# Optimization experiments

Measured on AMD Instinct MI355X. Metric: run time of the kernel, lower is better.

Reference implementation:

```python
import jax, jax.numpy as jnp
import numpy as np

L, D, H, d = 16, 1024, 16, 64
NB, BS = 1024, 16        # num physical blocks, block size (tokens per block)
START_POS = 16368        # T = START_POS + L = 16384
SCALE = 1.0 / np.sqrt(d)


def setup_inputs() -> dict:
    key = jax.random.key(0)
    ks = jax.random.split(key, 5)
    return {
        "x": jax.random.normal(ks[0], (L, D), jnp.float32),
        "k_pool": jax.random.normal(ks[1], (NB, BS, H, d), jnp.float32),
        "v_pool": jax.random.normal(ks[2], (NB, BS, H, d), jnp.float32),
        "W_attn": jax.random.normal(ks[3], (D, 3 * D), jnp.float32) * 0.02,
        "b_attn": jnp.zeros((3 * D,), jnp.float32),
        "W_proj": jax.random.normal(ks[4], (D, D), jnp.float32) * 0.02,
        "b_proj": jnp.zeros((D,), jnp.float32),
        "block_ids": jnp.arange(NB, dtype=jnp.int64),
        "start_pos": START_POS,
    }


def reference(x, k_pool, v_pool, W_attn, b_attn, W_proj, b_proj, block_ids, start_pos):
    # QKV projection
    qkv = x @ W_attn + b_attn                      # [L, 3D]
    q, k, v = jnp.split(qkv, 3, axis=-1)
    q = q.reshape(L, H, d)
    k = k.reshape(L, H, d)
    v = v.reshape(L, H, d)

    # paged write of new K/V into the pool
    pos = start_pos + jnp.arange(L)                # logical positions of new tokens
    blk = block_ids[pos // BS]                     # physical block per token
    off = pos % BS
    k_pool = k_pool.at[blk, off].set(k)
    v_pool = v_pool.at[blk, off].set(v)

    # paged read of the full prefix [0, T)
    T = start_pos + L
    k_pos = jnp.arange(T)
    kb = block_ids[k_pos // BS]
    ko = k_pos % BS
    k_cache = k_pool[kb, ko]                       # [T, H, d]
    v_cache = v_pool[kb, ko]                       # [T, H, d]

    # attention: scores [H, L, T]
    scores = jnp.einsum("lhd,thd->hlt", q, k_cache) * SCALE
    mask = k_pos[None, :] > pos[:, None]           # [L, T] future positions
    scores = jnp.where(mask[None, :, :], -jnp.inf, scores)
    attn = jax.nn.softmax(scores.astype(jnp.float32), axis=-1).astype(scores.dtype)

    out = jnp.einsum("hlt,thd->lhd", attn, v_cache).reshape(L, D)
    return out @ W_proj + b_proj
```

## Files before the change

### kernel.cpp

```cpp
#include <hip/hip_runtime.h>
#include <math.h>

#define L_TOK 16
#define DMODEL 1024
#define NHEAD 16
#define DHEAD 64
#define NBLK 1024
#define BSZ 16
#define START_POS_C 16368
#define TTOT 16384
#define SPLITS 128
#define CHUNK 128
#define KSPLIT 16
#define QSCALE (0.125f * 1.4426950408889634f)

#define OFF_QKVP 0
#define OFF_QW   (OFF_QKVP + KSPLIT * L_TOK * 3 * DMODEL)
#define OFF_ACC  (OFF_QW + NHEAD * L_TOK * DHEAD)
#define OFF_M    (OFF_ACC + NHEAD * SPLITS * L_TOK * DHEAD)
#define OFF_SE   (OFF_M + NHEAD * SPLITS * L_TOK)
#define OFF_ATTN (OFF_SE + NHEAD * SPLITS * L_TOK)
#define OFF_PROJP (OFF_ATTN + L_TOK * DMODEL)

typedef _Float16 half2_t __attribute__((ext_vector_type(2)));
typedef _Float16 half4_t __attribute__((ext_vector_type(4)));
typedef _Float16 half8_t __attribute__((ext_vector_type(8)));
typedef float float4v __attribute__((ext_vector_type(4)));

union H8 { _Float16 h[8]; half8_t v; };
union H4 { _Float16 h[4]; half4_t v; };

__global__ __launch_bounds__(256) void gemm_part(const float* __restrict__ x,
                                                 const float* __restrict__ W,
                                                 float* __restrict__ part,
                                                 int ncols) {
    const int lane = threadIdx.x & 63;
    const int wv = threadIdx.x >> 6;
    const int n = blockIdx.x * 64 + lane;
    const int k0 = blockIdx.y * (DMODEL / KSPLIT);
    const float* xr = x + (size_t)(wv * 4) * DMODEL;
    float a0 = 0.f, a1 = 0.f, a2 = 0.f, a3 = 0.f;
#pragma unroll 8
    for (int k = k0; k < k0 + DMODEL / KSPLIT; ++k) {
        float w = W[(size_t)k * ncols + n];
        a0 = fmaf(xr[k], w, a0);
        a1 = fmaf(xr[DMODEL + k], w, a1);
        a2 = fmaf(xr[2 * DMODEL + k], w, a2);
        a3 = fmaf(xr[3 * DMODEL + k], w, a3);
    }
    size_t base = ((size_t)blockIdx.y * L_TOK + wv * 4) * ncols + n;
    part[base] = a0;
    part[base + (size_t)ncols] = a1;
    part[base + 2 * (size_t)ncols] = a2;
    part[base + 3 * (size_t)ncols] = a3;
}

__global__ __launch_bounds__(256) void qkv_reduce_scatter(const float* __restrict__ part,
                                                          const float* __restrict__ b_attn,
                                                          const int* __restrict__ block_ids,
                                                          float* __restrict__ qws,
                                                          float* __restrict__ kpool,
                                                          float* __restrict__ vpool) {
    int tid = blockIdx.x * 256 + threadIdx.x;
    int n = tid % (3 * DMODEL);
    int l = tid / (3 * DMODEL);
    float s = b_attn[n];
#pragma unroll
    for (int kb = 0; kb < KSPLIT; ++kb)
        s += part[((size_t)kb * L_TOK + l) * (3 * DMODEL) + n];
    int sec = n >> 10;
    int m = n & (DMODEL - 1);
    int h = m >> 6;
    int dd = m & 63;
    if (sec == 0) {
        qws[(h * L_TOK + l) * DHEAD + dd] = s * QSCALE;
    } else {
        int pos = START_POS_C + l;
        int blk = block_ids[pos >> 4];
        int off = pos & 15;
        size_t idx = (((size_t)blk * BSZ + off) * NHEAD + h) * DHEAD + dd;
        if (sec == 1) kpool[idx] = s;
        else          vpool[idx] = s;
    }
}

__global__ __launch_bounds__(64) void paged_attn(const float* __restrict__ kpool,
                                                 const float* __restrict__ vpool,
                                                 const int* __restrict__ block_ids,
                                                 const float* __restrict__ qws,
                                                 float* __restrict__ accws,
                                                 float* __restrict__ m_arr,
                                                 float* __restrict__ se_arr) {
    const int h = blockIdx.x;
    const int s = blockIdx.y;
    const int lane = threadIdx.x;
    const int c = lane & 15;
    const int quad = lane >> 4;

    __shared__ float VT[2][64][36];

    H8 qb0, qb1;
    {
        const float* qr = qws + ((size_t)(h * L_TOK + c)) * DHEAD + quad * 8;
        float4 q0 = *(const float4*)(qr);
        float4 q1 = *(const float4*)(qr + 4);
        float4 q2 = *(const float4*)(qr + 32);
        float4 q3 = *(const float4*)(qr + 36);
        qb0.h[0] = (_Float16)q0.x; qb0.h[1] = (_Float16)q0.y;
        qb0.h[2] = (_Float16)q0.z; qb0.h[3] = (_Float16)q0.w;
        qb0.h[4] = (_Float16)q1.x; qb0.h[5] = (_Float16)q1.y;
        qb0.h[6] = (_Float16)q1.z; qb0.h[7] = (_Float16)q1.w;
        qb1.h[0] = (_Float16)q2.x; qb1.h[1] = (_Float16)q2.y;
        qb1.h[2] = (_Float16)q2.z; qb1.h[3] = (_Float16)q2.w;
        qb1.h[4] = (_Float16)q3.x; qb1.h[5] = (_Float16)q3.y;
        qb1.h[6] = (_Float16)q3.z; qb1.h[7] = (_Float16)q3.w;
    }

    float4v acc[4];
#pragma unroll
    for (int i = 0; i < 4; ++i) acc[i] = (float4v){0.f, 0.f, 0.f, 0.f};
    float m_run = -INFINITY, se_run = 0.f;

    const int blk0 = s * (CHUNK / 16);

#pragma unroll 2
    for (int grp = 0; grp < CHUNK / 32; ++grp) {
        const int tb = s * CHUNK + grp * 32;
        const int buf = grp & 1;
        const int pb0 = block_ids[blk0 + 2 * grp];
        const int pb1 = block_ids[blk0 + 2 * grp + 1];

        const float* kr0 = kpool + (((size_t)pb0 * BSZ + c) * NHEAD + h) * DHEAD + quad * 8;
        const float* kr1 = kpool + (((size_t)pb1 * BSZ + c) * NHEAD + h) * DHEAD + quad * 8;
        const float* vr0 = vpool + (((size_t)pb0 * BSZ + c) * NHEAD + h) * DHEAD + quad * 8;
        const float* vr1 = vpool + (((size_t)pb1 * BSZ + c) * NHEAD + h) * DHEAD + quad * 8;
        float4 k0a = *(const float4*)(kr0);      float4 k0b = *(const float4*)(kr0 + 4);
        float4 k0c = *(const float4*)(kr0 + 32); float4 k0d = *(const float4*)(kr0 + 36);
        float4 k1a = *(const float4*)(kr1);      float4 k1b = *(const float4*)(kr1 + 4);
        float4 k1c = *(const float4*)(kr1 + 32); float4 k1d = *(const float4*)(kr1 + 36);
        float4 v0a = *(const float4*)(vr0);      float4 v0b = *(const float4*)(vr0 + 4);
        float4 v0c = *(const float4*)(vr0 + 32); float4 v0d = *(const float4*)(vr0 + 36);
        float4 v1a = *(const float4*)(vr1);      float4 v1b = *(const float4*)(vr1 + 4);
        float4 v1c = *(const float4*)(vr1 + 32); float4 v1d = *(const float4*)(vr1 + 36);

        {
            float* w0 = &VT[buf][quad * 8][c];
            w0[0*36]=v0a.x; w0[1*36]=v0a.y; w0[2*36]=v0a.z; w0[3*36]=v0a.w;
            w0[4*36]=v0b.x; w0[5*36]=v0b.y; w0[6*36]=v0b.z; w0[7*36]=v0b.w;
            float* w1 = &VT[buf][32 + quad * 8][c];
            w1[0*36]=v0c.x; w1[1*36]=v0c.y; w1[2*36]=v0c.z; w1[3*36]=v0c.w;
            w1[4*36]=v0d.x; w1[5*36]=v0d.y; w1[6*36]=v0d.z; w1[7*36]=v0d.w;
            float* w2 = &VT[buf][quad * 8][16 + c];
            w2[0*36]=v1a.x; w2[1*36]=v1a.y; w2[2*36]=v1a.z; w2[3*36]=v1a.w;
            w2[4*36]=v1b.x; w2[5*36]=v1b.y; w2[6*36]=v1b.z; w2[7*36]=v1b.w;
            float* w3 = &VT[buf][32 + quad * 8][16 + c];
            w3[0*36]=v1c.x; w3[1*36]=v1c.y; w3[2*36]=v1c.z; w3[3*36]=v1c.w;
            w3[4*36]=v1d.x; w3[5*36]=v1d.y; w3[6*36]=v1d.z; w3[7*36]=v1d.w;
        }

        const float4v z4 = {0.f, 0.f, 0.f, 0.f};
        H8 ka, kb;
        ka.h[0]=(_Float16)k0a.x; ka.h[1]=(_Float16)k0a.y; ka.h[2]=(_Float16)k0a.z; ka.h[3]=(_Float16)k0a.w;
        ka.h[4]=(_Float16)k0b.x; ka.h[5]=(_Float16)k0b.y; ka.h[6]=(_Float16)k0b.z; ka.h[7]=(_Float16)k0b.w;
        kb.h[0]=(_Float16)k0c.x; kb.h[1]=(_Float16)k0c.y; kb.h[2]=(_Float16)k0c.z; kb.h[3]=(_Float16)k0c.w;
        kb.h[4]=(_Float16)k0d.x; kb.h[5]=(_Float16)k0d.y; kb.h[6]=(_Float16)k0d.z; kb.h[7]=(_Float16)k0d.w;
        float4v st0 = __builtin_amdgcn_mfma_f32_16x16x32_f16(ka.v, qb0.v, z4, 0, 0, 0);
        st0 = __builtin_amdgcn_mfma_f32_16x16x32_f16(kb.v, qb1.v, st0, 0, 0, 0);
        ka.h[0]=(_Float16)k1a.x; ka.h[1]=(_Float16)k1a.y; ka.h[2]=(_Float16)k1a.z; ka.h[3]=(_Float16)k1a.w;
        ka.h[4]=(_Float16)k1b.x; ka.h[5]=(_Float16)k1b.y; ka.h[6]=(_Float16)k1b.z; ka.h[7]=(_Float16)k1b.w;
        kb.h[0]=(_Float16)k1c.x; kb.h[1]=(_Float16)k1c.y; kb.h[2]=(_Float16)k1c.z; kb.h[3]=(_Float16)k1c.w;
        kb.h[4]=(_Float16)k1d.x; kb.h[5]=(_Float16)k1d.y; kb.h[6]=(_Float16)k1d.z; kb.h[7]=(_Float16)k1d.w;
        float4v st1 = __builtin_amdgcn_mfma_f32_16x16x32_f16(ka.v, qb0.v, z4, 0, 0, 0);
        st1 = __builtin_amdgcn_mfma_f32_16x16x32_f16(kb.v, qb1.v, st1, 0, 0, 0);

        if (tb + 31 > START_POS_C) {
#pragma unroll
            for (int r = 0; r < 4; ++r) {
                if (tb + 4 * quad + r > START_POS_C + c)      st0[r] = -INFINITY;
                if (tb + 16 + 4 * quad + r > START_POS_C + c) st1[r] = -INFINITY;
            }
        }

        float tm = fmaxf(fmaxf(fmaxf(st0[0], st0[1]), fmaxf(st0[2], st0[3])),
                         fmaxf(fmaxf(st1[0], st1[1]), fmaxf(st1[2], st1[3])));
        tm = fmaxf(tm, __shfl_xor(tm, 16, 64));
        tm = fmaxf(tm, __shfl_xor(tm, 32, 64));
        const float m_new = fmaxf(m_run, tm);
        const float alpha = exp2f(m_run - m_new);
        float p[8];
        p[0] = exp2f(st0[0] - m_new); p[1] = exp2f(st0[1] - m_new);
        p[2] = exp2f(st0[2] - m_new); p[3] = exp2f(st0[3] - m_new);
        p[4] = exp2f(st1[0] - m_new); p[5] = exp2f(st1[1] - m_new);
        p[6] = exp2f(st1[2] - m_new); p[7] = exp2f(st1[3] - m_new);
        H4 pa0, pa1;
        pa0.h[0]=(_Float16)p[0]; pa0.h[1]=(_Float16)p[1];
        pa0.h[2]=(_Float16)p[2]; pa0.h[3]=(_Float16)p[3];
        pa1.h[0]=(_Float16)p[4]; pa1.h[1]=(_Float16)p[5];
        pa1.h[2]=(_Float16)p[6]; pa1.h[3]=(_Float16)p[7];
        float ts = ((float)pa0.h[0] + (float)pa0.h[1]) + ((float)pa0.h[2] + (float)pa0.h[3])
                 + ((float)pa1.h[0] + (float)pa1.h[1]) + ((float)pa1.h[2] + (float)pa1.h[3]);
        ts += __shfl_xor(ts, 16, 64);
        ts += __shfl_xor(ts, 32, 64);
        se_run = se_run * alpha + ts;
        m_run = m_new;

        float ar[4];
#pragma unroll
        for (int r = 0; r < 4; ++r) ar[r] = __shfl(alpha, quad * 4 + r, 64);
#pragma unroll
        for (int ndv = 0; ndv < 4; ++ndv)
#pragma unroll
            for (int r = 0; r < 4; ++r) acc[ndv][r] *= ar[r];

#pragma unroll
        for (int tau = 0; tau < 2; ++tau) {
            const half4_t pf = tau ? pa1.v : pa0.v;
#pragma unroll
            for (int ndv = 0; ndv < 4; ++ndv) {
                float4 vb = *(const float4*)&VT[buf][16 * ndv + c][16 * tau + 4 * quad];
                H4 bf;
                bf.h[0] = (_Float16)vb.x; bf.h[1] = (_Float16)vb.y;
                bf.h[2] = (_Float16)vb.z; bf.h[3] = (_Float16)vb.w;
                acc[ndv] = __builtin_amdgcn_mfma_f32_16x16x16f16(pf, bf.v, acc[ndv], 0, 0, 0);
            }
        }
    }

    const size_t ob = (size_t)(h * SPLITS + s) * L_TOK * DHEAD;
#pragma unroll
    for (int ndv = 0; ndv < 4; ++ndv)
#pragma unroll
        for (int r = 0; r < 4; ++r)
            accws[ob + (size_t)(4 * quad + r) * DHEAD + 16 * ndv + c] = acc[ndv][r];
    if (quad == 0) {
        const size_t mb = (size_t)(h * SPLITS + s) * L_TOK + c;
        m_arr[mb] = m_run;
        se_arr[mb] = se_run;
    }
}

__global__ __launch_bounds__(256) void combine(const float* __restrict__ accws,
                                               const float* __restrict__ m_arr,
                                               const float* __restrict__ se_arr,
                                               float* __restrict__ attnws) {
    const int h = blockIdx.x >> 4;
    const int l = blockIdx.x & 15;
    const int w = threadIdx.x >> 6;
    const int lane = threadIdx.x & 63;
    __shared__ float sm[4], sse[4], sacc[4][64];

    float M = -INFINITY, num = 0.f, den = 0.f;
#pragma unroll 4
    for (int s = w; s < SPLITS; s += 4) {
        const size_t idx = (size_t)(h * SPLITS + s) * L_TOK + l;
        const float ms = m_arr[idx];
        const float ses = se_arr[idx];
        const float a = accws[idx * DHEAD + lane];
        const float Mn = fmaxf(M, ms);
        const float c_old = exp2f(M - Mn);
        const float c_new = exp2f(ms - Mn);
        num = num * c_old + a * c_new;
        den = den * c_old + ses * c_new;
        M = Mn;
    }
    if (lane == 0) { sm[w] = M; sse[w] = den; }
    sacc[w][lane] = num;
    __syncthreads();
    if (w == 0) {
        const float M0 = fmaxf(fmaxf(sm[0], sm[1]), fmaxf(sm[2], sm[3]));
        float nn = 0.f, dd = 0.f;
#pragma unroll
        for (int i = 0; i < 4; ++i) {
            const float wgt = exp2f(sm[i] - M0);
            nn = fmaf(wgt, sacc[i][lane], nn);
            dd = fmaf(wgt, sse[i], dd);
        }
        attnws[(size_t)l * DMODEL + h * DHEAD + lane] = nn / dd;
    }
}

__global__ __launch_bounds__(256) void proj_reduce(const float* __restrict__ part,
                                                   const float* __restrict__ bias,
                                                   float* __restrict__ out) {
    int tid = blockIdx.x * 256 + threadIdx.x;
    int n = tid & (DMODEL - 1);
    int l = tid >> 10;
    float s = bias[n];
#pragma unroll
    for (int kb = 0; kb < KSPLIT; ++kb)
        s += part[((size_t)kb * L_TOK + l) * DMODEL + n];
    out[tid] = s;
}

extern "C" void kernel_launch(void* const* d_in, const int* in_sizes, int n_in,
                              void* d_out, int out_size, void* d_ws, size_t ws_size,
                              hipStream_t stream) {
    const float* x       = (const float*)d_in[0];
    float* kpool         = (float*)d_in[1];
    float* vpool         = (float*)d_in[2];
    const float* W_attn  = (const float*)d_in[3];
    const float* b_attn  = (const float*)d_in[4];
    const float* W_proj  = (const float*)d_in[5];
    const float* b_proj  = (const float*)d_in[6];
    const int* block_ids = (const int*)d_in[7];
    float* ws  = (float*)d_ws;
    float* out = (float*)d_out;

    gemm_part<<<dim3(48, KSPLIT), 256, 0, stream>>>(x, W_attn, ws + OFF_QKVP, 3 * DMODEL);
    qkv_reduce_scatter<<<192, 256, 0, stream>>>(ws + OFF_QKVP, b_attn, block_ids,
                                                ws + OFF_QW, kpool, vpool);
    paged_attn<<<dim3(NHEAD, SPLITS), 64, 0, stream>>>(kpool, vpool, block_ids,
                                                       ws + OFF_QW, ws + OFF_ACC,
                                                       ws + OFF_M, ws + OFF_SE);
    combine<<<NHEAD * L_TOK, 256, 0, stream>>>(ws + OFF_ACC, ws + OFF_M, ws + OFF_SE,
                                               ws + OFF_ATTN);
    gemm_part<<<dim3(16, KSPLIT), 256, 0, stream>>>(ws + OFF_ATTN, W_proj, ws + OFF_PROJP, DMODEL);
    proj_reduce<<<64, 256, 0, stream>>>(ws + OFF_PROJP, b_proj, out);
}
```

Measured before the change: 207.8 us.

## Split paged attention chunk across four waves and vectorize projection GEMM columns

The paged attention kernel now runs 256 threads per block. Each wave handles 32 tokens of the 128-token chunk, and the per-wave softmax partials are merged in shared memory, so the serial online-softmax loop over four groups goes away. V is loaded directly into registers in MFMA layout rather than transposed through LDS. The GEMM partial kernel now has each thread compute four output columns with float4 loads and stores, and the grid shrinks by a factor of four. This adds a __syncthreads and a shared-memory combine step, and uses uncoalesced strided scalar V loads.

New measurement: 206.6 us. About the same (-0.6%).

```diff
diff --git a/kernel.cpp b/kernel.cpp
--- a/kernel.cpp
+++ b/kernel.cpp
@@ -22,7 +22,6 @@
 #define OFF_ATTN (OFF_SE + NHEAD * SPLITS * L_TOK)
 #define OFF_PROJP (OFF_ATTN + L_TOK * DMODEL)
 
-typedef _Float16 half2_t __attribute__((ext_vector_type(2)));
 typedef _Float16 half4_t __attribute__((ext_vector_type(4)));
 typedef _Float16 half8_t __attribute__((ext_vector_type(8)));
 typedef float float4v __attribute__((ext_vector_type(4)));
@@ -36,23 +35,27 @@
                                                  int ncols) {
     const int lane = threadIdx.x & 63;
     const int wv = threadIdx.x >> 6;
-    const int n = blockIdx.x * 64 + lane;
+    const int n = blockIdx.x * 256 + lane * 4;
     const int k0 = blockIdx.y * (DMODEL / KSPLIT);
     const float* xr = x + (size_t)(wv * 4) * DMODEL;
-    float a0 = 0.f, a1 = 0.f, a2 = 0.f, a3 = 0.f;
-#pragma unroll 8
+    float4v a0 = {0.f,0.f,0.f,0.f}, a1 = a0, a2 = a0, a3 = a0;
+#pragma unroll 4
     for (int k = k0; k < k0 + DMODEL / KSPLIT; ++k) {
-        float w = W[(size_t)k * ncols + n];
-        a0 = fmaf(xr[k], w, a0);
-        a1 = fmaf(xr[DMODEL + k], w, a1);
-        a2 = fmaf(xr[2 * DMODEL + k], w, a2);
-        a3 = fmaf(xr[3 * DMODEL + k], w, a3);
+        float4v w4 = *(const float4v*)&W[(size_t)k * ncols + n];
+        float x0 = xr[k];
+        float x1 = xr[DMODEL + k];
+        float x2 = xr[2 * DMODEL + k];
+        float x3 = xr[3 * DMODEL + k];
+        a0 += w4 * x0;
+        a1 += w4 * x1;
+        a2 += w4 * x2;
+        a3 += w4 * x3;
     }
     size_t base = ((size_t)blockIdx.y * L_TOK + wv * 4) * ncols + n;
-    part[base] = a0;
-    part[base + (size_t)ncols] = a1;
-    part[base + 2 * (size_t)ncols] = a2;
-    part[base + 3 * (size_t)ncols] = a3;
+    *(float4v*)&part[base] = a0;
+    *(float4v*)&part[base + (size_t)ncols] = a1;
+    *(float4v*)&part[base + 2 * (size_t)ncols] = a2;
+    *(float4v*)&part[base + 3 * (size_t)ncols] = a3;
 }
 
 __global__ __launch_bounds__(256) void qkv_reduce_scatter(const float* __restrict__ part,
@@ -84,158 +87,140 @@
     }
 }
 
-__global__ __launch_bounds__(64) void paged_attn(const float* __restrict__ kpool,
-                                                 const float* __restrict__ vpool,
-                                                 const int* __restrict__ block_ids,
-                                                 const float* __restrict__ qws,
-                                                 float* __restrict__ accws,
-                                                 float* __restrict__ m_arr,
-                                                 float* __restrict__ se_arr) {
+__global__ __launch_bounds__(256, 4) void paged_attn(const float* __restrict__ kpool,
+                                                     const float* __restrict__ vpool,
+                                                     const int* __restrict__ block_ids,
+                                                     const float* __restrict__ qws,
+                                                     float* __restrict__ accws,
+                                                     float* __restrict__ m_arr,
+                                                     float* __restrict__ se_arr) {
     const int h = blockIdx.x;
     const int s = blockIdx.y;
-    const int lane = threadIdx.x;
+    const int tid = threadIdx.x;
+    const int w = tid >> 6;
+    const int lane = tid & 63;
     const int c = lane & 15;
     const int quad = lane >> 4;
 
-    __shared__ float VT[2][64][36];
-
-    H8 qb0, qb1;
+    __shared__ __align__(16) float sacc[4][16][68];
+    __shared__ float sm[4][16], sse[4][16];
+
+    const int pb0 = block_ids[s * 8 + 2 * w];
+    const int pb1 = block_ids[s * 8 + 2 * w + 1];
+    const int tb0 = s * CHUNK + w * 32;
+    const int tb1 = tb0 + 16;
+
+    const float* qr = qws + ((size_t)(h * L_TOK + c)) * DHEAD + quad * 8;
+    float4 q0 = *(const float4*)(qr);
+    float4 q1 = *(const float4*)(qr + 4);
+    float4 q2 = *(const float4*)(qr + 32);
+    float4 q3 = *(const float4*)(qr + 36);
+    const float* kr0 = kpool + (((size_t)pb0 * BSZ + c) * NHEAD + h) * DHEAD + quad * 8;
+    const float* kr1 = kpool + (((size_t)pb1 * BSZ + c) * NHEAD + h) * DHEAD + quad * 8;
+    float4 k0a = *(const float4*)(kr0);      float4 k0b = *(const float4*)(kr0 + 4);
+    float4 k0c = *(const float4*)(kr0 + 32); float4 k0d = *(const float4*)(kr0 + 36);
+    float4 k1a = *(const float4*)(kr1);      float4 k1b = *(const float4*)(kr1 + 4);
+    float4 k1c = *(const float4*)(kr1 + 32); float4 k1d = *(const float4*)(kr1 + 36);
+    float v0[4][4], v1[4][4];
     {
-        const float* qr = qws + ((size_t)(h * L_TOK + c)) * DHEAD + quad * 8;
-        float4 q0 = *(const float4*)(qr);
-        float4 q1 = *(const float4*)(qr + 4);
-        float4 q2 = *(const float4*)(qr + 32);
-        float4 q3 = *(const float4*)(qr + 36);
-        qb0.h[0] = (_Float16)q0.x; qb0.h[1] = (_Float16)q0.y;
-        qb0.h[2] = (_Float16)q0.z; qb0.h[3] = (_Float16)q0.w;
-        qb0.h[4] = (_Float16)q1.x; qb0.h[5] = (_Float16)q1.y;
-        qb0.h[6] = (_Float16)q1.z; qb0.h[7] = (_Float16)q1.w;
-        qb1.h[0] = (_Float16)q2.x; qb1.h[1] = (_Float16)q2.y;
-        qb1.h[2] = (_Float16)q2.z; qb1.h[3] = (_Float16)q2.w;
-        qb1.h[4] = (_Float16)q3.x; qb1.h[5] = (_Float16)q3.y;
-        qb1.h[6] = (_Float16)q3.z; qb1.h[7] = (_Float16)q3.w;
-    }
-
-    float4v acc[4];
-#pragma unroll
-    for (int i = 0; i < 4; ++i) acc[i] = (float4v){0.f, 0.f, 0.f, 0.f};
-    float m_run = -INFINITY, se_run = 0.f;
-
-    const int blk0 = s * (CHUNK / 16);
-
-#pragma unroll 2
-    for (int grp = 0; grp < CHUNK / 32; ++grp) {
-        const int tb = s * CHUNK + grp * 32;
-        const int buf = grp & 1;
-        const int pb0 = block_ids[blk0 + 2 * grp];
-        const int pb1 = block_ids[blk0 + 2 * grp + 1];
-
-        const float* kr0 = kpool + (((size_t)pb0 * BSZ + c) * NHEAD + h) * DHEAD + quad * 8;
-        const float* kr1 = kpool + (((size_t)pb1 * BSZ + c) * NHEAD + h) * DHEAD + quad * 8;
-        const float* vr0 = vpool + (((size_t)pb0 * BSZ + c) * NHEAD + h) * DHEAD + quad * 8;
-        const float* vr1 = vpool + (((size_t)pb1 * BSZ + c) * NHEAD + h) * DHEAD + quad * 8;
-        float4 k0a = *(const float4*)(kr0);      float4 k0b = *(const float4*)(kr0 + 4);
-        float4 k0c = *(const float4*)(kr0 + 32); float4 k0d = *(const float4*)(kr0 + 36);
-        float4 k1a = *(const float4*)(kr1);      float4 k1b = *(const float4*)(kr1 + 4);
-        float4 k1c = *(const float4*)(kr1 + 32); float4 k1d = *(const float4*)(kr1 + 36);
-        float4 v0a = *(const float4*)(vr0);      float4 v0b = *(const float4*)(vr0 + 4);
-        float4 v0c = *(const float4*)(vr0 + 32); float4 v0d = *(const float4*)(vr0 + 36);
-        float4 v1a = *(const float4*)(vr1);      float4 v1b = *(const float4*)(vr1 + 4);
-        float4 v1c = *(const float4*)(vr1 + 32); float4 v1d = *(const float4*)(vr1 + 36);
-
-        {
-            float* w0 = &VT[buf][quad * 8][c];
-            w0[0*36]=v0a.x; w0[1*36]=v0a.y; w0[2*36]=v0a.z; w0[3*36]=v0a.w;
-            w0[4*36]=v0b.x; w0[5*36]=v0b.y; w0[6*36]=v0b.z; w0[7*36]=v0b.w;
-            float* w1 = &VT[buf][32 + quad * 8][c];
-            w1[0*36]=v0c.x; w1[1*36]=v0c.y; w1[2*36]=v0c.z; w1[3*36]=v0c.w;
-            w1[4*36]=v0d.x; w1[5*36]=v0d.y; w1[6*36]=v0d.z; w1[7*36]=v0d.w;
-            float* w2 = &VT[buf][quad * 8][16 + c];
-            w2[0*36]=v1a.x; w2[1*36]=v1a.y; w2[2*36]=v1a.z; w2[3*36]=v1a.w;
-            w2[4*36]=v1b.x; w2[5*36]=v1b.y; w2[6*36]=v1b.z; w2[7*36]=v1b.w;
-            float* w3 = &VT[buf][32 + quad * 8][16 + c];
-            w3[0*36]=v1c.x; w3[1*36]=v1c.y; w3[2*36]=v1c.z; w3[3*36]=v1c.w;
-            w3[4*36]=v1d.x; w3[5*36]=v1d.y; w3[6*36]=v1d.z; w3[7*36]=v1d.w;
-        }
-
-        const float4v z4 = {0.f, 0.f, 0.f, 0.f};
-        H8 ka, kb;
-        ka.h[0]=(_Float16)k0a.x; ka.h[1]=(_Float16)k0a.y; ka.h[2]=(_Float16)k0a.z; ka.h[3]=(_Float16)k0a.w;
-        ka.h[4]=(_Float16)k0b.x; ka.h[5]=(_Float16)k0b.y; ka.h[6]=(_Float16)k0b.z; ka.h[7]=(_Float16)k0b.w;
-        kb.h[0]=(_Float16)k0c.x; kb.h[1]=(_Float16)k0c.y; kb.h[2]=(_Float16)k0c.z; kb.h[3]=(_Float16)k0c.w;
-        kb.h[4]=(_Float16)k0d.x; kb.h[5]=(_Float16)k0d.y; kb.h[6]=(_Float16)k0d.z; kb.h[7]=(_Float16)k0d.w;
-        float4v st0 = __builtin_amdgcn_mfma_f32_16x16x32_f16(ka.v, qb0.v, z4, 0, 0, 0);
-        st0 = __builtin_amdgcn_mfma_f32_16x16x32_f16(kb.v, qb1.v, st0, 0, 0, 0);
-        ka.h[0]=(_Float16)k1a.x; ka.h[1]=(_Float16)k1a.y; ka.h[2]=(_Float16)k1a.z; ka.h[3]=(_Float16)k1a.w;
-        ka.h[4]=(_Float16)k1b.x; ka.h[5]=(_Float16)k1b.y; ka.h[6]=(_Float16)k1b.z; ka.h[7]=(_Float16)k1b.w;
-        kb.h[0]=(_Float16)k1c.x; kb.h[1]=(_Float16)k1c.y; kb.h[2]=(_Float16)k1c.z; kb.h[3]=(_Float16)k1c.w;
-        kb.h[4]=(_Float16)k1d.x; kb.h[5]=(_Float16)k1d.y; kb.h[6]=(_Float16)k1d.z; kb.h[7]=(_Float16)k1d.w;
-        float4v st1 = __builtin_amdgcn_mfma_f32_16x16x32_f16(ka.v, qb0.v, z4, 0, 0, 0);
-        st1 = __builtin_amdgcn_mfma_f32_16x16x32_f16(kb.v, qb1.v, st1, 0, 0, 0);
-
-        if (tb + 31 > START_POS_C) {
-#pragma unroll
-            for (int r = 0; r < 4; ++r) {
-                if (tb + 4 * quad + r > START_POS_C + c)      st0[r] = -INFINITY;
-                if (tb + 16 + 4 * quad + r > START_POS_C + c) st1[r] = -INFINITY;
+        const float* vb0 = vpool + ((size_t)pb0 * BSZ * NHEAD + h) * DHEAD + c;
+        const float* vb1 = vpool + ((size_t)pb1 * BSZ * NHEAD + h) * DHEAD + c;
+#pragma unroll
+        for (int j = 0; j < 4; ++j) {
+            const float* r0 = vb0 + (size_t)(4 * quad + j) * (NHEAD * DHEAD);
+            const float* r1 = vb1 + (size_t)(4 * quad + j) * (NHEAD * DHEAD);
+#pragma unroll
+            for (int ndv = 0; ndv < 4; ++ndv) {
+                v0[j][ndv] = r0[16 * ndv];
+                v1[j][ndv] = r1[16 * ndv];
             }
         }
-
-        float tm = fmaxf(fmaxf(fmaxf(st0[0], st0[1]), fmaxf(st0[2], st0[3])),
-                         fmaxf(fmaxf(st1[0], st1[1]), fmaxf(st1[2], st1[3])));
-        tm = fmaxf(tm, __shfl_xor(tm, 16, 64));
-        tm = fmaxf(tm, __shfl_xor(tm, 32, 64));
-        const float m_new = fmaxf(m_run, tm);
-        const float alpha = exp2f(m_run - m_new);
-        float p[8];
-        p[0] = exp2f(st0[0] - m_new); p[1] = exp2f(st0[1] - m_new);
-        p[2] = exp2f(st0[2] - m_new); p[3] = exp2f(st0[3] - m_new);
-        p[4] = exp2f(st1[0] - m_new); p[5] = exp2f(st1[1] - m_new);
-        p[6] = exp2f(st1[2] - m_new); p[7] = exp2f(st1[3] - m_new);
-        H4 pa0, pa1;
-        pa0.h[0]=(_Float16)p[0]; pa0.h[1]=(_Float16)p[1];
-        pa0.h[2]=(_Float16)p[2]; pa0.h[3]=(_Float16)p[3];
-        pa1.h[0]=(_Float16)p[4]; pa1.h[1]=(_Float16)p[5];
-        pa1.h[2]=(_Float16)p[6]; pa1.h[3]=(_Float16)p[7];
-        float ts = ((float)pa0.h[0] + (float)pa0.h[1]) + ((float)pa0.h[2] + (float)pa0.h[3])
-                 + ((float)pa1.h[0] + (float)pa1.h[1]) + ((float)pa1.h[2] + (float)pa1.h[3]);
-        ts += __shfl_xor(ts, 16, 64);
-        ts += __shfl_xor(ts, 32, 64);
-        se_run = se_run * alpha + ts;
-        m_run = m_new;
-
-        float ar[4];
-#pragma unroll
-        for (int r = 0; r < 4; ++r) ar[r] = __shfl(alpha, quad * 4 + r, 64);
-#pragma unroll
-        for (int ndv = 0; ndv < 4; ++ndv)
-#pragma unroll
-            for (int r = 0; r < 4; ++r) acc[ndv][r] *= ar[r];
-
-#pragma unroll
-        for (int tau = 0; tau < 2; ++tau) {
-            const half4_t pf = tau ? pa1.v : pa0.v;
-#pragma unroll
-            for (int ndv = 0; ndv < 4; ++ndv) {
-                float4 vb = *(const float4*)&VT[buf][16 * ndv + c][16 * tau + 4 * quad];
-                H4 bf;
-                bf.h[0] = (_Float16)vb.x; bf.h[1] = (_Float16)vb.y;
-                bf.h[2] = (_Float16)vb.z; bf.h[3] = (_Float16)vb.w;
-                acc[ndv] = __builtin_amdgcn_mfma_f32_16x16x16f16(pf, bf.v, acc[ndv], 0, 0, 0);
-            }
-        }
-    }
-
-    const size_t ob = (size_t)(h * SPLITS + s) * L_TOK * DHEAD;
+    }
+
+    H8 qb0, qb1;
+    qb0.h[0]=(_Float16)q0.x; qb0.h[1]=(_Float16)q0.y; qb0.h[2]=(_Float16)q0.z; qb0.h[3]=(_Float16)q0.w;
+    qb0.h[4]=(_Float16)q1.x; qb0.h[5]=(_Float16)q1.y; qb0.h[6]=(_Float16)q1.z; qb0.h[7]=(_Float16)q1.w;
+    qb1.h[0]=(_Float16)q2.x; qb1.h[1]=(_Float16)q2.y; qb1.h[2]=(_Float16)q2.z; qb1.h[3]=(_Float16)q2.w;
+    qb1.h[4]=(_Float16)q3.x; qb1.h[5]=(_Float16)q3.y; qb1.h[6]=(_Float16)q3.z; qb1.h[7]=(_Float16)q3.w;
+
+    const float4v z4 = {0.f, 0.f, 0.f, 0.f};
+    H8 ka, kb;
+    ka.h[0]=(_Float16)k0a.x; ka.h[1]=(_Float16)k0a.y; ka.h[2]=(_Float16)k0a.z; ka.h[3]=(_Float16)k0a.w;
+    ka.h[4]=(_Float16)k0b.x; ka.h[5]=(_Float16)k0b.y; ka.h[6]=(_Float16)k0b.z; ka.h[7]=(_Float16)k0b.w;
+    kb.h[0]=(_Float16)k0c.x; kb.h[1]=(_Float16)k0c.y; kb.h[2]=(_Float16)k0c.z; kb.h[3]=(_Float16)k0c.w;
+    kb.h[4]=(_Float16)k0d.x; kb.h[5]=(_Float16)k0d.y; kb.h[6]=(_Float16)k0d.z; kb.h[7]=(_Float16)k0d.w;
+    float4v st0 = __builtin_amdgcn_mfma_f32_16x16x32_f16(ka.v, qb0.v, z4, 0, 0, 0);
+    st0 = __builtin_amdgcn_mfma_f32_16x16x32_f16(kb.v, qb1.v, st0, 0, 0, 0);
+    ka.h[0]=(_Float16)k1a.x; ka.h[1]=(_Float16)k1a.y; ka.h[2]=(_Float16)k1a.z; ka.h[3]=(_Float16)k1a.w;
+    ka.h[4]=(_Float16)k1b.x; ka.h[5]=(_Float16)k1b.y; ka.h[6]=(_Float16)k1b.z; ka.h[7]=(_Float16)k1b.w;
+    kb.h[0]=(_Float16)k1c.x; kb.h[1]=(_Float16)k1c.y; kb.h[2]=(_Float16)k1c.z; kb.h[3]=(_Float16)k1c.w;
+    kb.h[4]=(_Float16)k1d.x; kb.h[5]=(_Float16)k1d.y; kb.h[6]=(_Float16)k1d.z; kb.h[7]=(_Float16)k1d.w;
+    float4v st1 = __builtin_amdgcn_mfma_f32_16x16x32_f16(ka.v, qb0.v, z4, 0, 0, 0);
+    st1 = __builtin_amdgcn_mfma_f32_16x16x32_f16(kb.v, qb1.v, st1, 0, 0, 0);
+
+    if (tb0 + 15 > START_POS_C) {
+#pragma unroll
+        for (int r = 0; r < 4; ++r)
+            if (tb0 + 4 * quad + r > START_POS_C + c) st0[r] = -INFINITY;
+    }
+    if (tb1 + 15 > START_POS_C) {
+#pragma unroll
+        for (int r = 0; r < 4; ++r)
+            if (tb1 + 4 * quad + r > START_POS_C + c) st1[r] = -INFINITY;
+    }
+
+    float tm = fmaxf(fmaxf(fmaxf(st0[0], st0[1]), fmaxf(st0[2], st0[3])),
+                     fmaxf(fmaxf(st1[0], st1[1]), fmaxf(st1[2], st1[3])));
+    tm = fmaxf(tm, __shfl_xor(tm, 16, 64));
+    tm = fmaxf(tm, __shfl_xor(tm, 32, 64));
+    H4 pa0, pa1;
+    pa0.h[0]=(_Float16)exp2f(st0[0]-tm); pa0.h[1]=(_Float16)exp2f(st0[1]-tm);
+    pa0.h[2]=(_Float16)exp2f(st0[2]-tm); pa0.h[3]=(_Float16)exp2f(st0[3]-tm);
+    pa1.h[0]=(_Float16)exp2f(st1[0]-tm); pa1.h[1]=(_Float16)exp2f(st1[1]-tm);
+    pa1.h[2]=(_Float16)exp2f(st1[2]-tm); pa1.h[3]=(_Float16)exp2f(st1[3]-tm);
+    float ts = ((float)pa0.h[0] + (float)pa0.h[1]) + ((float)pa0.h[2] + (float)pa0.h[3])
+             + ((float)pa1.h[0] + (float)pa1.h[1]) + ((float)pa1.h[2] + (float)pa1.h[3]);
+    ts += __shfl_xor(ts, 16, 64);
+    ts += __shfl_xor(ts, 32, 64);
+
+    float4v acc[4];
+#pragma unroll
+    for (int i = 0; i < 4; ++i) acc[i] = z4;
+#pragma unroll
+    for (int ndv = 0; ndv < 4; ++ndv) {
+        H4 bf;
+        bf.h[0]=(_Float16)v0[0][ndv]; bf.h[1]=(_Float16)v0[1][ndv];
+        bf.h[2]=(_Float16)v0[2][ndv]; bf.h[3]=(_Float16)v0[3][ndv];
+        acc[ndv] = __builtin_amdgcn_mfma_f32_16x16x16f16(pa0.v, bf.v, acc[ndv], 0, 0, 0);
+        bf.h[0]=(_Float16)v1[0][ndv]; bf.h[1]=(_Float16)v1[1][ndv];
+        bf.h[2]=(_Float16)v1[2][ndv]; bf.h[3]=(_Float16)v1[3][ndv];
+        acc[ndv] = __builtin_amdgcn_mfma_f32_16x16x16f16(pa1.v, bf.v, acc[ndv], 0, 0, 0);
+    }
+
 #pragma unroll
     for (int ndv = 0; ndv < 4; ++ndv)
 #pragma unroll
         for (int r = 0; r < 4; ++r)
-            accws[ob + (size_t)(4 * quad + r) * DHEAD + 16 * ndv + c] = acc[ndv][r];
-    if (quad == 0) {
-        const size_t mb = (size_t)(h * SPLITS + s) * L_TOK + c;
-        m_arr[mb] = m_run;
-        se_arr[mb] = se_run;
+            sacc[w][4 * quad + r][16 * ndv + c] = acc[ndv][r];
+    if (quad == 0) { sm[w][c] = tm; sse[w][c] = ts; }
+    __syncthreads();
+
+    const int q = tid >> 4;
+    const int dseg = tid & 15;
+    float m0 = sm[0][q], m1 = sm[1][q], m2 = sm[2][q], m3 = sm[3][q];
+    float M = fmaxf(fmaxf(m0, m1), fmaxf(m2, m3));
+    float u0 = exp2f(m0 - M), u1 = exp2f(m1 - M), u2 = exp2f(m2 - M), u3 = exp2f(m3 - M);
+    float den = u0 * sse[0][q] + u1 * sse[1][q] + u2 * sse[2][q] + u3 * sse[3][q];
+    float4v num = u0 * (*(const float4v*)&sacc[0][q][4 * dseg])
+                + u1 * (*(const float4v*)&sacc[1][q][4 * dseg])
+                + u2 * (*(const float4v*)&sacc[2][q][4 * dseg])
+                + u3 * (*(const float4v*)&sacc[3][q][4 * dseg]);
+    const size_t ob = ((size_t)(h * SPLITS + s) * L_TOK + q) * DHEAD + 4 * dseg;
+    *(float4v*)&accws[ob] = num;
+    if (dseg == 0) {
+        const size_t mb = (size_t)(h * SPLITS + s) * L_TOK + q;
+        m_arr[mb] = M;
+        se_arr[mb] = den;
     }
 }
 
@@ -306,14 +291,14 @@
     float* ws  = (float*)d_ws;
     float* out = (float*)d_out;
 
-    gemm_part<<<dim3(48, KSPLIT), 256, 0, stream>>>(x, W_attn, ws + OFF_QKVP, 3 * DMODEL);
+    gemm_part<<<dim3(12, KSPLIT), 256, 0, stream>>>(x, W_attn, ws + OFF_QKVP, 3 * DMODEL);
     qkv_reduce_scatter<<<192, 256, 0, stream>>>(ws + OFF_QKVP, b_attn, block_ids,
                                                 ws + OFF_QW, kpool, vpool);
-    paged_attn<<<dim3(NHEAD, SPLITS), 64, 0, stream>>>(kpool, vpool, block_ids,
-                                                       ws + OFF_QW, ws + OFF_ACC,
-                                                       ws + OFF_M, ws + OFF_SE);
+    paged_attn<<<dim3(NHEAD, SPLITS), 256, 0, stream>>>(kpool, vpool, block_ids,
+                                                        ws + OFF_QW, ws + OFF_ACC,
+                                                        ws + OFF_M, ws + OFF_SE);
     combine<<<NHEAD * L_TOK, 256, 0, stream>>>(ws + OFF_ACC, ws + OFF_M, ws + OFF_SE,
                                                ws + OFF_ATTN);
-    gemm_part<<<dim3(16, KSPLIT), 256, 0, stream>>>(ws + OFF_ATTN, W_proj, ws + OFF_PROJP, DMODEL);
+    gemm_part<<<dim3(4, KSPLIT), 256, 0, stream>>>(ws + OFF_ATTN, W_proj, ws + OFF_PROJP, DMODEL);
     proj_reduce<<<64, 256, 0, stream>>>(ws + OFF_PROJP, b_proj, out);
 }
```
